# Kernel tuning notes

Hardware: AMD Instinct MI355X
Metric: run time of the kernel (lower is better)

The kernel has to match this reference:

```python
import jax, jax.numpy as jnp
import numpy as np

H, D = 16, 64  # n_heads, head_dim


def l2norm(t):
    # F.normalize(t, p=2, dim=-1)
    return t / jnp.maximum(jnp.linalg.norm(t, axis=-1, keepdims=True), 1e-12)


def setup_inputs() -> dict:
    key = jax.random.key(0)
    ks = jax.random.split(key, 6)
    B, N, C = 2, 2048, 1024
    x = jax.random.normal(ks[0], (B, N, C), jnp.float32)
    pos_bias = jax.random.normal(ks[1], (1, H, N, N), jnp.float32)
    mask = jnp.zeros((B, 1, 1, N), bool)  # attn_mask: True = masked
    Wqkv = jax.random.normal(ks[2], (C, 3 * H * D), jnp.float32) / np.sqrt(C)
    Wout = jax.random.normal(ks[3], (H * D, C), jnp.float32) / np.sqrt(H * D)
    Wpre = jax.random.normal(ks[4], (H, H), jnp.float32) / np.sqrt(H)   # 1x1 conv pre
    bpre = jnp.zeros((H,), jnp.float32)
    Wpost = jax.random.normal(ks[5], (H, H), jnp.float32) / np.sqrt(H)  # 1x1 conv post
    bpost = jnp.zeros((H,), jnp.float32)
    temperature = jnp.float32(15.5)
    return {"x": x, "pos_bias": pos_bias, "mask": mask, "Wqkv": Wqkv,
            "Wout": Wout, "Wpre": Wpre, "bpre": bpre, "Wpost": Wpost,
            "bpost": bpost, "temperature": temperature}


def reference(x, pos_bias, mask, Wqkv, Wout, Wpre, bpre, Wpost, bpost, temperature):
    B, N, C = x.shape
    # qkv: 'b n (h d qkv) -> qkv b h n d'
    qkv = (x @ Wqkv).reshape(B, N, H, D, 3)
    q = jnp.transpose(qkv[..., 0], (0, 2, 1, 3))  # [B,H,N,D]
    k = jnp.transpose(qkv[..., 1], (0, 2, 1, 3))
    v = jnp.transpose(qkv[..., 2], (0, 2, 1, 3))
    q, k = l2norm(q), l2norm(k)  # cosine_sim
    kv = jnp.stack([k, v], axis=0)  # attach_cache with cache=None
    # temperature-scaled cosine-sim scores
    dots = jnp.einsum('bhid,bhjd->bhij', q, k) * temperature
    # talking heads pre (1x1 conv over head channel)
    dots = jnp.einsum('gh,bhij->bgij', Wpre, dots) + bpre[None, :, None, None]
    dots = dots + pos_bias
    dots = jnp.where(mask, -jnp.finfo(dots.dtype).max, dots)
    attn = jax.nn.softmax(dots, axis=-1)
    # talking heads post
    attn = jnp.einsum('gh,bhij->bgij', Wpost, attn) + bpost[None, :, None, None]
    out = jnp.einsum('bhij,bhjd->bhid', attn, v)  # [B,H,N,D]
    out = jnp.transpose(out, (0, 2, 1, 3)).reshape(B, N, H * D) @ Wout
    return (out, kv)
```

## Files before the change

### kernel.cpp

```cpp
#include <hip/hip_runtime.h>
#include <hip/hip_fp16.h>
#include <stdint.h>

typedef __attribute__((ext_vector_type(8))) short bf16x8;
typedef __attribute__((ext_vector_type(4))) float f32x4;
typedef __attribute__((ext_vector_type(4))) short short4v;

#define DEV __device__ __forceinline__
#define L2E 1.4426950408889634f

DEV float bf2f(unsigned short s){ union{unsigned int u; float f;} x; x.u = ((unsigned int)s)<<16; return x.f; }
DEV unsigned short f2bf(float f){ union{float f; unsigned int u;} x; x.f = f; x.u += 0x7fffu + ((x.u>>16)&1u); return (unsigned short)(x.u>>16); }
DEV float h2f(unsigned short u){ return __half2float(__ushort_as_half(u)); }
DEV unsigned short f2h(float f){ return __half_as_ushort(__float2half(f)); }

DEV f32x4 mfma16(bf16x8 a, bf16x8 b, f32x4 c){
  return __builtin_amdgcn_mfma_f32_16x16x32_bf16(a, b, c, 0, 0, 0);
}
DEV f32x4 zero4(){ f32x4 z; z[0]=0.f; z[1]=0.f; z[2]=0.f; z[3]=0.f; return z; }
DEV bf16x8 zerob(){ bf16x8 z; z[0]=0;z[1]=0;z[2]=0;z[3]=0;z[4]=0;z[5]=0;z[6]=0;z[7]=0; return z; }
DEV float fexp2(float x){ float r; asm volatile("v_exp_f32 %0, %1" : "=v"(r) : "v"(x)); return r; }
DEV void barw(){ asm volatile("s_waitcnt lgkmcnt(0)" ::: "memory"); __builtin_amdgcn_s_barrier(); }

__global__ __launch_bounds__(256) void k_f32_to_bf16(const float* __restrict__ in, unsigned short* __restrict__ out, int n4){
  int i = blockIdx.x*256 + threadIdx.x;
  if (i < n4){
    float4 v = ((const float4*)in)[i];
    short4v o; o.x=(short)f2bf(v.x); o.y=(short)f2bf(v.y); o.z=(short)f2bf(v.z); o.w=(short)f2bf(v.w);
    ((short4v*)out)[i] = o;
  }
}

__global__ __launch_bounds__(256) void k_convT(const float* __restrict__ in, unsigned short* __restrict__ out, int R, int Cc){
  __shared__ float t[32][33];
  int c0 = blockIdx.x*32, r0 = blockIdx.y*32;
  int tid = threadIdx.x;
  int row = tid>>3, col4 = (tid&7)*4;
  float4 v = *(const float4*)&in[(size_t)(r0+row)*Cc + c0 + col4];
  t[row][col4+0]=v.x; t[row][col4+1]=v.y; t[row][col4+2]=v.z; t[row][col4+3]=v.w;
  __syncthreads();
  short4v o;
  o.x=(short)f2bf(t[col4+0][row]); o.y=(short)f2bf(t[col4+1][row]);
  o.z=(short)f2bf(t[col4+2][row]); o.w=(short)f2bf(t[col4+3][row]);
  *(short4v*)&out[(size_t)(c0+row)*R + r0 + col4] = o;
}

__global__ __launch_bounds__(256) void k_prep(const float* __restrict__ wpre, const float* __restrict__ wpost,
                                              const float* __restrict__ temp,
                                              unsigned short* __restrict__ wpre_t2,
                                              unsigned short* __restrict__ wpost_b){
  int t = threadIdx.x;
  float T = temp[0];
  wpre_t2[t] = f2bf(wpre[t]*T*L2E);
  wpost_b[t] = f2bf(wpost[t]);
}

__global__ __launch_bounds__(256) void k_maskf(const unsigned char* __restrict__ mask, float* __restrict__ maskf){
  int i = blockIdx.x*256 + threadIdx.x;
  if (i < 4096) maskf[i] = mask[i] ? -1e30f : 0.f;
}

__global__ __launch_bounds__(256) void k_pbexp(const float* __restrict__ pb, unsigned short* __restrict__ epb){
  int idx = blockIdx.x*256 + threadIdx.x;
  int i = idx >> 9, j4 = (idx & 511)*4;
  float4 v[16];
  #pragma unroll
  for (int g=0; g<16; ++g)
    v[g] = *(const float4*)&pb[(size_t)g*4194304 + (size_t)i*2048 + j4];
  #pragma unroll
  for (int jj=0; jj<4; ++jj){
    unsigned int pk[8];
    #pragma unroll
    for (int g2=0; g2<8; ++g2){
      float a = fexp2(((const float*)&v[2*g2  ])[jj] * L2E);
      float b = fexp2(((const float*)&v[2*g2+1])[jj] * L2E);
      pk[g2] = (unsigned int)f2h(a) | ((unsigned int)f2h(b)<<16);
    }
    uint4 o0, o1;
    o0.x=pk[0]; o0.y=pk[1]; o0.z=pk[2]; o0.w=pk[3];
    o1.x=pk[4]; o1.y=pk[5]; o1.z=pk[6]; o1.w=pk[7];
    *(uint4*)&epb[((size_t)idx*4 + jj)*16]     = o0;
    *(uint4*)&epb[((size_t)idx*4 + jj)*16 + 8] = o1;
  }
}

template<int OUTF>
__global__ __launch_bounds__(256,2) void k_gemm(const unsigned short* __restrict__ A, const unsigned short* __restrict__ Bt,
                                                void* __restrict__ Cv, int M, int Nn, int K){
  __shared__ unsigned short As[128][72];
  __shared__ unsigned short Bs[128][72];
  int tid = threadIdx.x;
  int n0 = blockIdx.x*128, m0 = blockIdx.y*128;
  int w = tid>>6, lane = tid&63, lg = lane>>4, lp = lane&15;
  int wm = (w>>1)*64, wn = (w&1)*64;
  f32x4 acc[4][4];
  #pragma unroll
  for (int i=0;i<4;++i)
    #pragma unroll
    for (int j=0;j<4;++j) acc[i][j] = zero4();

  for (int kt=0; kt<K; kt+=64){
    #pragma unroll
    for (int cch=0; cch<4; ++cch){
      int e = tid + cch*256; int r = e>>3, cl = (e&7)*8;
      *(bf16x8*)&As[r][cl] = *(const bf16x8*)&A[(size_t)(m0+r)*K + kt + cl];
      *(bf16x8*)&Bs[r][cl] = *(const bf16x8*)&Bt[(size_t)(n0+r)*K + kt + cl];
    }
    __syncthreads();
    #pragma unroll
    for (int ks=0; ks<2; ++ks){
      bf16x8 a[4], b[4];
      #pragma unroll
      for (int mi=0; mi<4; ++mi) a[mi] = *(const bf16x8*)&As[wm+mi*16+lp][ks*32 + lg*8];
      #pragma unroll
      for (int ni=0; ni<4; ++ni) b[ni] = *(const bf16x8*)&Bs[wn+ni*16+lp][ks*32 + lg*8];
      #pragma unroll
      for (int mi=0; mi<4; ++mi)
        #pragma unroll
        for (int ni=0; ni<4; ++ni)
          acc[mi][ni] = mfma16(a[mi], b[ni], acc[mi][ni]);
    }
    __syncthreads();
  }
  #pragma unroll
  for (int mi=0; mi<4; ++mi)
    #pragma unroll
    for (int ni=0; ni<4; ++ni)
      #pragma unroll
      for (int r=0; r<4; ++r){
        int row = m0+wm+mi*16+lg*4+r, col = n0+wn+ni*16+lp;
        if (OUTF) ((float*)Cv)[(size_t)row*Nn+col] = acc[mi][ni][r];
        else ((unsigned short*)Cv)[(size_t)row*Nn+col] = f2bf(acc[mi][ni][r]);
      }
}

__global__ __launch_bounds__(256) void k_split_norm(const unsigned short* __restrict__ qkv,
                                                    unsigned short* __restrict__ q, unsigned short* __restrict__ k,
                                                    unsigned short* __restrict__ v, float* __restrict__ kv_out){
  int w = threadIdx.x>>6, lane = threadIdx.x&63;
  int widx = blockIdx.x*4 + w;
  int h = widx & 15; int bn = widx >> 4;
  int b = bn >> 11; int n = bn & 2047;
  size_t base = (size_t)bn*3072 + h*192 + lane*3;
  float qv = bf2f(qkv[base]), kvv = bf2f(qkv[base+1]), vv = bf2f(qkv[base+2]);
  float nq = qv*qv, nk = kvv*kvv;
  #pragma unroll
  for (int m=1; m<64; m<<=1){ nq += __shfl_xor(nq, m); nk += __shfl_xor(nk, m); }
  float qn = qv / fmaxf(sqrtf(nq), 1e-12f);
  float kn = kvv / fmaxf(sqrtf(nk), 1e-12f);
  size_t idx = ((size_t)(b*16+h)*2048 + n)*64 + lane;
  q[idx] = f2bf(qn); k[idx] = f2bf(kn); v[idx] = f2bf(vv);
  kv_out[idx] = kn;
  kv_out[4194304 + idx] = vv;
}

__global__ __launch_bounds__(256) void k_transpose_v(const unsigned short* __restrict__ v, unsigned short* __restrict__ vt){
  __shared__ unsigned short t[64][72];
  int bh = blockIdx.y; int n0 = blockIdx.x*64;
  int tid = threadIdx.x;
  #pragma unroll
  for (int cch=0; cch<2; ++cch){
    int e = tid + cch*256; int r = e>>3, c8 = (e&7)*8;
    *(bf16x8*)&t[r][c8] = *(const bf16x8*)&v[((size_t)bh*2048 + n0 + r)*64 + c8];
  }
  __syncthreads();
  #pragma unroll
  for (int cch=0; cch<2; ++cch){
    int e = tid + cch*256; int d = e>>3, nn8 = (e&7)*8;
    bf16x8 o;
    #pragma unroll
    for (int i=0;i<8;++i) o[i] = (short)t[nn8+i][d];
    *(bf16x8*)&vt[((size_t)bh*64 + d)*2048 + n0 + nn8] = o;
  }
}

__global__ __launch_bounds__(256) void k_vsum(const unsigned short* __restrict__ v, float* __restrict__ vsum){
  int bg = blockIdx.x;
  int d = threadIdx.x & 63, part = threadIdx.x>>6;
  float s = 0.f;
  for (int n = part*512; n < part*512+512; ++n) s += bf2f(v[((size_t)bg*2048 + n)*64 + d]);
  __shared__ float red[4][64];
  red[part][d] = s; __syncthreads();
  if (part==0) vsum[bg*64 + d] = red[0][d]+red[1][d]+red[2][d]+red[3][d];
}

__global__ __launch_bounds__(512,4) void k_score2(
    const unsigned short* __restrict__ q,
    const unsigned short* __restrict__ kk,
    const unsigned short* __restrict__ epb,
    const float* __restrict__ maskf,
    const unsigned short* __restrict__ wpre_t2,
    const float* __restrict__ bpre,
    unsigned short* __restrict__ Pb,
    float* __restrict__ part_l)
{
  __shared__ __align__(16) char smem[40960];
  const int tid = threadIdx.x;
  const int w = tid>>6, lane = tid&63, lg = lane>>4, lp = lane&15;
  const int bid = blockIdx.x;
  const int qd = bid>>4, r2 = bid&15;
  const int b = r2>>3, n = qd*8 + (r2&7);
  const int it = n>>2, js = n&3;
  const int i0 = it*16, jsb = js*512;
  const int mbase = b*2048;

  bf16x8 qf[2][2];
  #pragma unroll
  for (int hh=0; hh<2; ++hh){
    const unsigned short* qb = q + ((size_t)(b*16+2*w+hh)*2048 + i0 + lp)*64;
    qf[hh][0] = *(const bf16x8*)(qb + lg*8);
    qf[hh][1] = *(const bf16x8*)(qb + 32 + lg*8);
  }
  bf16x8 preA = zerob();
  if (lg < 2) preA = *(const bf16x8*)&wpre_t2[lp*16 + lg*8];
  float bpre_s[4];
  #pragma unroll
  for (int r=0;r<4;++r) bpre_s[r] = bpre[lg*4+r]*L2E - 32.0f;

  float sacc[2][4];
  #pragma unroll
  for (int ii=0;ii<2;++ii)
    #pragma unroll
    for (int r=0;r<4;++r) sacc[ii][r] = 0.f;

  const size_t kbase0 = (size_t)(b*16 + 2*w)*131072;
  const size_t kbase1 = (size_t)(b*16 + 2*w+1)*131072;

  bf16x8 k0v[4], k1v[4];
  #pragma unroll
  for (int kf=0; kf<2; ++kf)
    #pragma unroll
    for (int jf=0; jf<2; ++jf){
      size_t off = (size_t)(jsb + jf*16 + lp)*64 + kf*32 + lg*8;
      k0v[kf*2+jf] = *(const bf16x8*)(kk + kbase0 + off);
      k1v[kf*2+jf] = *(const bf16x8*)(kk + kbase1 + off);
    }

  for (int t=0; t<16; ++t){
    const int j0 = jsb + t*32;
    const int j0n = jsb + ((t+1)&15)*32;
    char* sbuf = smem + (t&1)*20480;

    short4v ept[4];
    #pragma unroll
    for (int cc=0; cc<4; ++cc){
      int il = 2*w + (cc>>1);
      ept[cc] = *(const short4v*)&epb[(((size_t)(i0+il)*2048) + j0 + (cc&1)*16 + lp)*16 + lg*4];
    }
    float mk0 = maskf[mbase + j0 + lp];
    float mk1 = maskf[mbase + j0 + 16 + lp];

    f32x4 s0[2], s1[2];
    #pragma unroll
    for (int jf=0;jf<2;++jf){ s0[jf]=zero4(); s1[jf]=zero4(); }
    #pragma unroll
    for (int kf=0; kf<2; ++kf)
      #pragma unroll
      for (int jf=0; jf<2; ++jf){
        s0[jf] = mfma16(qf[0][kf], k0v[kf*2+jf], s0[jf]);
        s1[jf] = mfma16(qf[1][kf], k1v[kf*2+jf], s1[jf]);
      }
    #pragma unroll
    for (int jf=0;jf<2;++jf)
      #pragma unroll
      for (int r=0;r<4;++r){
        int ij = (lg*4+r)*32 + jf*16 + lp;
        unsigned int pk = (unsigned int)f2bf(s0[jf][r]) | ((unsigned int)f2bf(s1[jf][r])<<16);
        *(unsigned int*)(sbuf + ij*40 + w*4) = pk;
      }
    #pragma unroll
    for (int kf=0; kf<2; ++kf)
      #pragma unroll
      for (int jf=0; jf<2; ++jf){
        size_t off = (size_t)(j0n + jf*16 + lp)*64 + kf*32 + lg*8;
        k0v[kf*2+jf] = *(const bf16x8*)(kk + kbase0 + off);
        k1v[kf*2+jf] = *(const bf16x8*)(kk + kbase1 + off);
      }
    barw();

    #pragma unroll
    for (int cc=0; cc<4; ++cc){
      int c = w*4+cc;
      int il = 2*w + (cc>>1);
      int jl = (cc&1)*16 + lp;
      bf16x8 sfrag = zerob();
      if (lg < 2) sfrag = *(const bf16x8*)(sbuf + (c*16+lp)*40 + lg*16);
      f32x4 pa = mfma16(preA, sfrag, zero4());
      float mkj = (cc&1) ? mk1 : mk0;
      float pv0 = fexp2(pa[0] + bpre_s[0] + mkj) * h2f((unsigned short)ept[cc][0]);
      float pv1 = fexp2(pa[1] + bpre_s[1] + mkj) * h2f((unsigned short)ept[cc][1]);
      float pv2 = fexp2(pa[2] + bpre_s[2] + mkj) * h2f((unsigned short)ept[cc][2]);
      float pv3 = fexp2(pa[3] + bpre_s[3] + mkj) * h2f((unsigned short)ept[cc][3]);
      sacc[cc>>1][0] += pv0; sacc[cc>>1][1] += pv1;
      sacc[cc>>1][2] += pv2; sacc[cc>>1][3] += pv3;
      short4v p4;
      p4.x = (short)f2bf(pv0); p4.y = (short)f2bf(pv1);
      p4.z = (short)f2bf(pv2); p4.w = (short)f2bf(pv3);
      *(short4v*)&Pb[(((size_t)(b*2048 + i0+il)*2048) + j0 + jl)*16 + lg*4] = p4;
    }
  }

  #pragma unroll
  for (int ii=0;ii<2;++ii)
    #pragma unroll
    for (int r=0;r<4;++r){
      float v = sacc[ii][r];
      #pragma unroll
      for (int m=1; m<16; m<<=1) v += __shfl_xor(v, m);
      sacc[ii][r] = v;
    }
  if (lp == 0){
    int base = ((b*128+it)*4 + js)*256;
    #pragma unroll
    for (int ii=0;ii<2;++ii){
      float4 st; st.x = sacc[ii][0]; st.y = sacc[ii][1]; st.z = sacc[ii][2]; st.w = sacc[ii][3];
      *(float4*)&part_l[base + (2*w+ii)*16 + lg*4] = st;
    }
  }
}

__global__ __launch_bounds__(512,4) void k_mix(
    const unsigned short* __restrict__ Pb,
    const unsigned short* __restrict__ vt,
    const unsigned short* __restrict__ wpost_b,
    const float* __restrict__ bpost,
    const float* __restrict__ vsum,
    const float* __restrict__ part_l,
    float* __restrict__ pout0,
    float* __restrict__ pout1)
{
  __shared__ __align__(16) char smem[33792];
  float* linv = (float*)(smem + 32768);
  const int tid = threadIdx.x;
  const int w = tid>>6, lane = tid&63, lg = lane>>4, lp = lane&15;
  const int bid = blockIdx.x;
  const int qd = bid>>4, r2 = bid&15;
  const int b = r2>>3, n = qd*8 + (r2&7);
  const int it = n>>1, js = n&1;
  const int i0 = it*16, jsb = js*1024;

  if (tid < 256){
    int base = ((b*128+it)*4)*256 + tid;
    float sum = part_l[base] + part_l[base+256] + part_l[base+512] + part_l[base+768];
    linv[tid] = 1.f/sum;
  }
  __syncthreads();

  bf16x8 postB[2];
  #pragma unroll
  for (int ii=0;ii<2;++ii){
    postB[ii] = zerob();
    if (lg < 2){
      bf16x8 wf = *(const bf16x8*)&wpost_b[lp*16 + lg*8];
      int i = 2*w+ii;
      #pragma unroll
      for (int e=0;e<8;++e){
        float vsc = bf2f((unsigned short)wf[e]) * linv[i*16 + lg*8 + e];
        postB[ii][e] = (short)f2bf(vsc);
      }
    }
  }

  f32x4 oacc[2][4];
  #pragma unroll
  for (int hh=0; hh<2; ++hh)
    #pragma unroll
    for (int df=0; df<4; ++df) oacc[hh][df] = zero4();

  __syncthreads();

  for (int t=0; t<32; ++t){
    const int j0 = jsb + t*32;
    char* abuf = smem + (t&1)*16384;
    bf16x8 pfr[4];
    #pragma unroll
    for (int cc=0; cc<4; ++cc){
      int il = 2*w + (cc>>1);
      pfr[cc] = zerob();
      if (lg < 2)
        pfr[cc] = *(const bf16x8*)&Pb[(((size_t)(b*2048 + i0+il)*2048) + j0 + (cc&1)*16 + lp)*16 + lg*8];
    }
    bf16x8 vfr[2][4];
    #pragma unroll
    for (int hh=0; hh<2; ++hh)
      #pragma unroll
      for (int df=0; df<4; ++df)
        vfr[hh][df] = *(const bf16x8*)(vt + ((size_t)(b*16+2*w+hh)*64 + df*16 + lp)*2048 + j0 + lg*8);
    #pragma unroll
    for (int cc=0; cc<4; ++cc){
      int il = 2*w + (cc>>1);
      f32x4 aa = mfma16(pfr[cc], postB[cc>>1], zero4());
      short4v av;
      av.x = (short)f2bf(aa[0]); av.y = (short)f2bf(aa[1]);
      av.z = (short)f2bf(aa[2]); av.w = (short)f2bf(aa[3]);
      int row = lp*16 + il;
      int chunk = ((cc&1)*4 + lg) ^ ((lp ^ il)&6);
      *(short4v*)(abuf + row*64 + chunk*8) = av;
    }
    barw();
    #pragma unroll
    for (int hh=0; hh<2; ++hh){
      int gg = 2*w+hh;
      bf16x8 af = *(const bf16x8*)(abuf + (gg*16+lp)*64 + (((lg*2) ^ ((gg^lp)&6))*8));
      #pragma unroll
      for (int df=0; df<4; ++df)
        oacc[hh][df] = mfma16(af, vfr[hh][df], oacc[hh][df]);
    }
  }

  float* po = js ? pout1 : pout0;
  #pragma unroll
  for (int hh=0; hh<2; ++hh){
    int gg = 2*w+hh;
    float bp = (js==0) ? bpost[gg] : 0.f;
    #pragma unroll
    for (int df=0; df<4; ++df){
      int d = df*16+lp;
      float vs = vsum[(b*16+gg)*64 + d];
      #pragma unroll
      for (int r=0;r<4;++r){
        po[((size_t)b*2048 + i0 + lg*4 + r)*1024 + gg*64 + d] = oacc[hh][df][r] + bp*vs;
      }
    }
  }
}

__global__ __launch_bounds__(256) void k_combine(const float* __restrict__ p0, const float* __restrict__ p1,
                                                 unsigned short* __restrict__ ao){
  int i = blockIdx.x*256 + threadIdx.x;
  float4 a = ((const float4*)p0)[i];
  float4 c = ((const float4*)p1)[i];
  short4v o;
  o.x=(short)f2bf(a.x+c.x); o.y=(short)f2bf(a.y+c.y);
  o.z=(short)f2bf(a.z+c.z); o.w=(short)f2bf(a.w+c.w);
  ((short4v*)ao)[i] = o;
}

extern "C" void kernel_launch(void* const* d_in, const int* in_sizes, int n_in,
                              void* d_out, int out_size, void* d_ws, size_t ws_size,
                              hipStream_t stream)
{
  const float* x        = (const float*)d_in[0];
  const float* pos_bias = (const float*)d_in[1];
  const unsigned char* mask = (const unsigned char*)d_in[2];
  const float* Wqkv     = (const float*)d_in[3];
  const float* Wout     = (const float*)d_in[4];
  const float* Wpre     = (const float*)d_in[5];
  const float* bpre     = (const float*)d_in[6];
  const float* Wpost    = (const float*)d_in[7];
  const float* bpost    = (const float*)d_in[8];
  const float* temp     = (const float*)d_in[9];
  float* out = (float*)d_out;
  float* kv_out = out + 4194304;

  char* ws = (char*)d_ws;
  unsigned short* XB    = (unsigned short*)(ws + 0);
  unsigned short* WT    = (unsigned short*)(ws + 8388608);
  unsigned short* WOT   = (unsigned short*)(ws + 8388608);
  float*          PART_L= (float*)        (ws + 11534336);
  unsigned short* WPRE2 = (unsigned short*)(ws + 12583424);
  unsigned short* WPOST = (unsigned short*)(ws + 12583936);
  float*          VSUM  = (float*)        (ws + 12584448);
  float*          MASKF = (float*)        (ws + 12593152);
  unsigned short* QKV   = (unsigned short*)(ws + 14680064);
  unsigned short* VT    = (unsigned short*)(ws + 14680064);
  float*          POUT0 = (float*)        (ws + 23068672);
  unsigned short* Q     = (unsigned short*)(ws + 39845888);
  unsigned short* KB    = (unsigned short*)(ws + 48234496);
  unsigned short* VB    = (unsigned short*)(ws + 56623104);
  float*          POUT1 = (float*)        (ws + 56623104);
  unsigned short* PB    = (unsigned short*)(ws + 75497472);
  unsigned short* EPB   = (unsigned short*)(ws + 343932928);
  unsigned short* AO    = XB;

  k_f32_to_bf16<<<4096, 256, 0, stream>>>(x, XB, 1048576);
  k_convT<<<dim3(96,32), 256, 0, stream>>>(Wqkv, WT, 1024, 3072);
  k_gemm<0><<<dim3(24,32), 256, 0, stream>>>(XB, WT, (void*)QKV, 4096, 3072, 1024);
  k_split_norm<<<16384, 256, 0, stream>>>(QKV, Q, KB, VB, kv_out);
  k_transpose_v<<<dim3(32,32), 256, 0, stream>>>(VB, VT);
  k_vsum<<<32, 256, 0, stream>>>(VB, VSUM);
  k_prep<<<1, 256, 0, stream>>>(Wpre, Wpost, temp, WPRE2, WPOST);
  k_maskf<<<16, 256, 0, stream>>>(mask, MASKF);
  k_convT<<<dim3(32,32), 256, 0, stream>>>(Wout, WOT, 1024, 1024);

  k_pbexp<<<4096, 256, 0, stream>>>(pos_bias, EPB);
  k_score2<<<1024, 512, 0, stream>>>(Q, KB, EPB, MASKF, WPRE2, bpre, PB, PART_L);
  k_mix<<<512, 512, 0, stream>>>(PB, VT, WPOST, bpost, VSUM, PART_L, POUT0, POUT1);
  k_combine<<<4096, 256, 0, stream>>>(POUT0, POUT1, AO);
  k_gemm<1><<<dim3(8,32), 256, 0, stream>>>(AO, WOT, d_out, 4096, 1024, 1024);
}
```

Baseline: 580.3 us.

## Read pos_bias directly in score kernel and drop split-K mix with combine

Removes the precomputed exp(pos_bias) fp16 buffer: the score kernel now loads fp32 pos_bias directly and folds it into the exponent argument with an fma. The mix kernel no longer splits the key range in two, so each block loops over all 2048 keys and writes bf16 output directly, eliminating the fp32 partial buffers and the combine kernel. This saves an extra pass over the large pos_bias tensor and the partial-output traffic. The cost is strided, uncoalesced-per-head fp32 pos_bias loads inside the score loop and half as many mix blocks, each doing twice the work, which lowers parallelism.

After: 521.4 us. -10.2%, faster.

```diff
diff --git a/kernel.cpp b/kernel.cpp
--- a/kernel.cpp
+++ b/kernel.cpp
@@ -1,5 +1,4 @@
 #include <hip/hip_runtime.h>
-#include <hip/hip_fp16.h>
 #include <stdint.h>
 
 typedef __attribute__((ext_vector_type(8))) short bf16x8;
@@ -11,8 +10,6 @@
 
 DEV float bf2f(unsigned short s){ union{unsigned int u; float f;} x; x.u = ((unsigned int)s)<<16; return x.f; }
 DEV unsigned short f2bf(float f){ union{float f; unsigned int u;} x; x.f = f; x.u += 0x7fffu + ((x.u>>16)&1u); return (unsigned short)(x.u>>16); }
-DEV float h2f(unsigned short u){ return __half2float(__ushort_as_half(u)); }
-DEV unsigned short f2h(float f){ return __half_as_ushort(__float2half(f)); }
 
 DEV f32x4 mfma16(bf16x8 a, bf16x8 b, f32x4 c){
   return __builtin_amdgcn_mfma_f32_16x16x32_bf16(a, b, c, 0, 0, 0);
@@ -60,30 +57,6 @@
   if (i < 4096) maskf[i] = mask[i] ? -1e30f : 0.f;
 }
 
-__global__ __launch_bounds__(256) void k_pbexp(const float* __restrict__ pb, unsigned short* __restrict__ epb){
-  int idx = blockIdx.x*256 + threadIdx.x;
-  int i = idx >> 9, j4 = (idx & 511)*4;
-  float4 v[16];
-  #pragma unroll
-  for (int g=0; g<16; ++g)
-    v[g] = *(const float4*)&pb[(size_t)g*4194304 + (size_t)i*2048 + j4];
-  #pragma unroll
-  for (int jj=0; jj<4; ++jj){
-    unsigned int pk[8];
-    #pragma unroll
-    for (int g2=0; g2<8; ++g2){
-      float a = fexp2(((const float*)&v[2*g2  ])[jj] * L2E);
-      float b = fexp2(((const float*)&v[2*g2+1])[jj] * L2E);
-      pk[g2] = (unsigned int)f2h(a) | ((unsigned int)f2h(b)<<16);
-    }
-    uint4 o0, o1;
-    o0.x=pk[0]; o0.y=pk[1]; o0.z=pk[2]; o0.w=pk[3];
-    o1.x=pk[4]; o1.y=pk[5]; o1.z=pk[6]; o1.w=pk[7];
-    *(uint4*)&epb[((size_t)idx*4 + jj)*16]     = o0;
-    *(uint4*)&epb[((size_t)idx*4 + jj)*16 + 8] = o1;
-  }
-}
-
 template<int OUTF>
 __global__ __launch_bounds__(256,2) void k_gemm(const unsigned short* __restrict__ A, const unsigned short* __restrict__ Bt,
                                                 void* __restrict__ Cv, int M, int Nn, int K){
@@ -184,10 +157,10 @@
   if (part==0) vsum[bg*64 + d] = red[0][d]+red[1][d]+red[2][d]+red[3][d];
 }
 
-__global__ __launch_bounds__(512,4) void k_score2(
+__global__ __launch_bounds__(512,4) void k_score(
     const unsigned short* __restrict__ q,
     const unsigned short* __restrict__ kk,
-    const unsigned short* __restrict__ epb,
+    const float* __restrict__ pos_bias,
     const float* __restrict__ maskf,
     const unsigned short* __restrict__ wpre_t2,
     const float* __restrict__ bpre,
@@ -202,7 +175,6 @@
   const int b = r2>>3, n = qd*8 + (r2&7);
   const int it = n>>2, js = n&3;
   const int i0 = it*16, jsb = js*512;
-  const int mbase = b*2048;
 
   bf16x8 qf[2][2];
   #pragma unroll
@@ -240,15 +212,17 @@
     const int j0 = jsb + t*32;
     const int j0n = jsb + ((t+1)&15)*32;
     char* sbuf = smem + (t&1)*20480;
-
-    short4v ept[4];
+    float pbt[4][4];
     #pragma unroll
     for (int cc=0; cc<4; ++cc){
       int il = 2*w + (cc>>1);
-      ept[cc] = *(const short4v*)&epb[(((size_t)(i0+il)*2048) + j0 + (cc&1)*16 + lp)*16 + lg*4];
-    }
-    float mk0 = maskf[mbase + j0 + lp];
-    float mk1 = maskf[mbase + j0 + 16 + lp];
+      int jl = (cc&1)*16 + lp;
+      #pragma unroll
+      for (int r=0;r<4;++r)
+        pbt[cc][r] = pos_bias[(size_t)(lg*4+r)*4194304 + (size_t)(i0+il)*2048 + j0 + jl];
+    }
+    float mk0 = maskf[b*2048 + j0 + lp];
+    float mk1 = maskf[b*2048 + j0 + 16 + lp];
 
     f32x4 s0[2], s1[2];
     #pragma unroll
@@ -287,10 +261,10 @@
       if (lg < 2) sfrag = *(const bf16x8*)(sbuf + (c*16+lp)*40 + lg*16);
       f32x4 pa = mfma16(preA, sfrag, zero4());
       float mkj = (cc&1) ? mk1 : mk0;
-      float pv0 = fexp2(pa[0] + bpre_s[0] + mkj) * h2f((unsigned short)ept[cc][0]);
-      float pv1 = fexp2(pa[1] + bpre_s[1] + mkj) * h2f((unsigned short)ept[cc][1]);
-      float pv2 = fexp2(pa[2] + bpre_s[2] + mkj) * h2f((unsigned short)ept[cc][2]);
-      float pv3 = fexp2(pa[3] + bpre_s[3] + mkj) * h2f((unsigned short)ept[cc][3]);
+      float pv0 = fexp2(fmaf(pbt[cc][0], L2E, pa[0] + bpre_s[0] + mkj));
+      float pv1 = fexp2(fmaf(pbt[cc][1], L2E, pa[1] + bpre_s[1] + mkj));
+      float pv2 = fexp2(fmaf(pbt[cc][2], L2E, pa[2] + bpre_s[2] + mkj));
+      float pv3 = fexp2(fmaf(pbt[cc][3], L2E, pa[3] + bpre_s[3] + mkj));
       sacc[cc>>1][0] += pv0; sacc[cc>>1][1] += pv1;
       sacc[cc>>1][2] += pv2; sacc[cc>>1][3] += pv3;
       short4v p4;
@@ -326,18 +300,15 @@
     const float* __restrict__ bpost,
     const float* __restrict__ vsum,
     const float* __restrict__ part_l,
-    float* __restrict__ pout0,
-    float* __restrict__ pout1)
+    unsigned short* __restrict__ ao)
 {
   __shared__ __align__(16) char smem[33792];
   float* linv = (float*)(smem + 32768);
   const int tid = threadIdx.x;
   const int w = tid>>6, lane = tid&63, lg = lane>>4, lp = lane&15;
   const int bid = blockIdx.x;
-  const int qd = bid>>4, r2 = bid&15;
-  const int b = r2>>3, n = qd*8 + (r2&7);
-  const int it = n>>1, js = n&1;
-  const int i0 = it*16, jsb = js*1024;
+  const int b = bid & 1, it = bid >> 1;
+  const int i0 = it*16;
 
   if (tid < 256){
     int base = ((b*128+it)*4)*256 + tid;
@@ -369,8 +340,8 @@
 
   __syncthreads();
 
-  for (int t=0; t<32; ++t){
-    const int j0 = jsb + t*32;
+  for (int t=0; t<64; ++t){
+    const int j0 = t*32;
     char* abuf = smem + (t&1)*16384;
     bf16x8 pfr[4];
     #pragma unroll
@@ -408,32 +379,21 @@
     }
   }
 
-  float* po = js ? pout1 : pout0;
   #pragma unroll
   for (int hh=0; hh<2; ++hh){
     int gg = 2*w+hh;
-    float bp = (js==0) ? bpost[gg] : 0.f;
+    float bp = bpost[gg];
     #pragma unroll
     for (int df=0; df<4; ++df){
       int d = df*16+lp;
       float vs = vsum[(b*16+gg)*64 + d];
       #pragma unroll
       for (int r=0;r<4;++r){
-        po[((size_t)b*2048 + i0 + lg*4 + r)*1024 + gg*64 + d] = oacc[hh][df][r] + bp*vs;
-      }
-    }
-  }
-}
-
-__global__ __launch_bounds__(256) void k_combine(const float* __restrict__ p0, const float* __restrict__ p1,
-                                                 unsigned short* __restrict__ ao){
-  int i = blockIdx.x*256 + threadIdx.x;
-  float4 a = ((const float4*)p0)[i];
-  float4 c = ((const float4*)p1)[i];
-  short4v o;
-  o.x=(short)f2bf(a.x+c.x); o.y=(short)f2bf(a.y+c.y);
-  o.z=(short)f2bf(a.z+c.z); o.w=(short)f2bf(a.w+c.w);
-  ((short4v*)ao)[i] = o;
+        float o = oacc[hh][df][r] + bp*vs;
+        ao[((size_t)(b*2048 + i0 + lg*4 + r))*1024 + gg*64 + d] = f2bf(o);
+      }
+    }
+  }
 }
 
 extern "C" void kernel_launch(void* const* d_in, const int* in_sizes, int n_in,
@@ -464,13 +424,10 @@
   float*          MASKF = (float*)        (ws + 12593152);
   unsigned short* QKV   = (unsigned short*)(ws + 14680064);
   unsigned short* VT    = (unsigned short*)(ws + 14680064);
-  float*          POUT0 = (float*)        (ws + 23068672);
   unsigned short* Q     = (unsigned short*)(ws + 39845888);
   unsigned short* KB    = (unsigned short*)(ws + 48234496);
   unsigned short* VB    = (unsigned short*)(ws + 56623104);
-  float*          POUT1 = (float*)        (ws + 56623104);
   unsigned short* PB    = (unsigned short*)(ws + 75497472);
-  unsigned short* EPB   = (unsigned short*)(ws + 343932928);
   unsigned short* AO    = XB;
 
   k_f32_to_bf16<<<4096, 256, 0, stream>>>(x, XB, 1048576);
@@ -483,9 +440,7 @@
   k_maskf<<<16, 256, 0, stream>>>(mask, MASKF);
   k_convT<<<dim3(32,32), 256, 0, stream>>>(Wout, WOT, 1024, 1024);
 
-  k_pbexp<<<4096, 256, 0, stream>>>(pos_bias, EPB);
-  k_score2<<<1024, 512, 0, stream>>>(Q, KB, EPB, MASKF, WPRE2, bpre, PB, PART_L);
-  k_mix<<<512, 512, 0, stream>>>(PB, VT, WPOST, bpost, VSUM, PART_L, POUT0, POUT1);
-  k_combine<<<4096, 256, 0, stream>>>(POUT0, POUT1, AO);
+  k_score<<<1024, 512, 0, stream>>>(Q, KB, pos_bias, MASKF, WPRE2, bpre, PB, PART_L);
+  k_mix<<<256, 512, 0, stream>>>(PB, VT, WPOST, bpost, VSUM, PART_L, AO);
   k_gemm<1><<<dim3(8,32), 256, 0, stream>>>(AO, WOT, d_out, 4096, 1024, 1024);
 }
```
